# Kernel optimization log

Measured on AMD Instinct MI355X. Metric: run time of the kernel, lower is better.

The kernel has to match this reference:

```python
import jax, jax.numpy as jnp
import numpy as np


def dense_image_warp(img, flow):
    """Faithful port of tfa.image.dense_image_warp(img, flow):
    output[b,i,j] = bilinear_sample(img[b], (i - flow[b,i,j,0], j - flow[b,i,j,1]))
    with floors clamped to [0, size-2] and alphas clipped to [0,1] (TFA semantics).
    """
    B, H, W, C = img.shape
    gy = jnp.arange(H, dtype=flow.dtype)[None, :, None]   # [1,H,1]
    gx = jnp.arange(W, dtype=flow.dtype)[None, None, :]   # [1,1,W]
    # query = grid - flow
    qy = gy - flow[..., 0]                                 # [B,H,W]
    qx = gx - flow[..., 1]
    fy = jnp.clip(jnp.floor(qy), 0.0, H - 2)
    fx = jnp.clip(jnp.floor(qx), 0.0, W - 2)
    ay = jnp.clip(qy - fy, 0.0, 1.0)[..., None]            # [B,H,W,1]
    ax = jnp.clip(qx - fx, 0.0, 1.0)[..., None]
    fy_i = fy.astype(jnp.int32)
    fx_i = fx.astype(jnp.int32)

    flat = img.reshape(B, H * W, C)

    def gather(yy, xx):  # yy,xx: [B,H,W] int32
        idx = (yy * W + xx).reshape(B, H * W, 1)
        return jnp.take_along_axis(flat, idx, axis=1).reshape(B, H, W, C)

    tl = gather(fy_i,     fx_i)
    tr = gather(fy_i,     fx_i + 1)
    bl = gather(fy_i + 1, fx_i)
    br = gather(fy_i + 1, fx_i + 1)

    top = tl + (tr - tl) * ax
    bot = bl + (br - bl) * ax
    return top + (bot - top) * ay


def setup_inputs() -> dict:
    key = jax.random.key(0)
    k1, k2 = jax.random.split(key)
    img = jax.random.normal(k1, (16, 256, 512, 32), dtype=jnp.float32)
    flow = jax.random.normal(k2, (16, 256, 512, 2), dtype=jnp.float32)
    return {"img": img, "flow": flow}


def reference(img, flow):
    # InvWarpFlow.call: dense_image_warp(img, -flow)
    return dense_image_warp(img, -flow)
```

## Files before the change

kernel.cpp:

```cpp
#include <hip/hip_runtime.h>


__global__ __launch_bounds__(256) void InvWarpFlow_kernel(
    const float* __restrict__ img,
    const float* __restrict__ flow,
    float* __restrict__ out)
{
    constexpr int H = 256, W = 512, C = 32;
    int t   = blockIdx.x * blockDim.x + threadIdx.x;
    int cg  = t & 7;
    int pix = t >> 3;
    int x   = pix & (W - 1);
    int yb  = pix >> 9;
    int y   = yb & (H - 1);
    int b   = yb >> 8;

    const float2 f = *reinterpret_cast<const float2*>(flow + (size_t)pix * 2);
    float qy = (float)y + f.x;
    float qx = (float)x + f.y;

    float fy = fminf(fmaxf(floorf(qy), 0.0f), (float)(H - 2));
    float fx = fminf(fmaxf(floorf(qx), 0.0f), (float)(W - 2));
    float ay = fminf(fmaxf(qy - fy, 0.0f), 1.0f);
    float ax = fminf(fmaxf(qx - fx, 0.0f), 1.0f);
    int iy = (int)fy;
    int ix = (int)fx;

    const float* base = img + ((((size_t)b * H + iy) * W + ix) * C) + cg * 4;
    float4 tl = *reinterpret_cast<const float4*>(base);
    float4 tr = *reinterpret_cast<const float4*>(base + C);
    float4 bl = *reinterpret_cast<const float4*>(base + (size_t)W * C);
    float4 br = *reinterpret_cast<const float4*>(base + (size_t)W * C + C);

    float4 o;
    {
        float top, bot;
        top = tl.x + (tr.x - tl.x) * ax;
        bot = bl.x + (br.x - bl.x) * ax;
        o.x = top + (bot - top) * ay;
        top = tl.y + (tr.y - tl.y) * ax;
        bot = bl.y + (br.y - bl.y) * ax;
        o.y = top + (bot - top) * ay;
        top = tl.z + (tr.z - tl.z) * ax;
        bot = bl.z + (br.z - bl.z) * ax;
        o.z = top + (bot - top) * ay;
        top = tl.w + (tr.w - tl.w) * ax;
        bot = bl.w + (br.w - bl.w) * ax;
        o.w = top + (bot - top) * ay;
    }

    *reinterpret_cast<float4*>(out + (size_t)pix * C + cg * 4) = o;
}

extern "C" void kernel_launch(void* const* d_in, const int* in_sizes, int n_in,
                              void* d_out, int out_size, void* d_ws, size_t ws_size,
                              hipStream_t stream) {
    const float* img  = (const float*)d_in[0];
    const float* flow = (const float*)d_in[1];
    float* out = (float*)d_out;

    constexpr int B = 16, H = 256, W = 512;
    int total_threads = B * H * W * 8;
    int block = 256;
    int grid  = total_threads / block;
    InvWarpFlow_kernel<<<grid, block, 0, stream>>>(img, flow, out);
}
```

Measured before the change: 114.6 us.

## Tile pixels into 8x8 blocks with XCD-aware block remapping and nontemporal stores

```diff
diff --git a/kernel.cpp b/kernel.cpp
--- a/kernel.cpp
+++ b/kernel.cpp
@@ -1,19 +1,37 @@
 #include <hip/hip_runtime.h>
 
 
-__global__ __launch_bounds__(256) void InvWarpFlow_kernel(
+typedef float floatx4 __attribute__((ext_vector_type(4)));
+
+__global__ __launch_bounds__(512) void InvWarpFlow_kernel(
     const float* __restrict__ img,
     const float* __restrict__ flow,
     float* __restrict__ out)
 {
     constexpr int H = 256, W = 512, C = 32;
-    int t   = blockIdx.x * blockDim.x + threadIdx.x;
-    int cg  = t & 7;
-    int pix = t >> 3;
-    int x   = pix & (W - 1);
-    int yb  = pix >> 9;
-    int y   = yb & (H - 1);
-    int b   = yb >> 8;
+    constexpr int TW = 8, TH = 8;
+    constexpr int TILES_Y = H / TH;
+    constexpr int TILES_X = W / TW;
+    constexpr int NBLK = 16 * TILES_X * TILES_Y;
+    constexpr int PER_XCD = NBLK / 8;
+
+    int bid = blockIdx.x;
+    int logical = (bid & 7) * PER_XCD + (bid >> 3);
+
+    int ty   = logical & (TILES_Y - 1);
+    int rest = logical >> 5;
+    int tx   = rest & (TILES_X - 1);
+    int b    = rest >> 6;
+
+    int t  = threadIdx.x;
+    int cg = t & 7;
+    int p  = t >> 3;
+    int lx = p & 7;
+    int ly = p >> 3;
+
+    int x = tx * TW + lx;
+    int y = ty * TH + ly;
+    int pix = ((b << 8) + y) * W + x;
 
     const float2 f = *reinterpret_cast<const float2*>(flow + (size_t)pix * 2);
     float qy = (float)y + f.x;
@@ -27,29 +45,16 @@
     int ix = (int)fx;
 
     const float* base = img + ((((size_t)b * H + iy) * W + ix) * C) + cg * 4;
-    float4 tl = *reinterpret_cast<const float4*>(base);
-    float4 tr = *reinterpret_cast<const float4*>(base + C);
-    float4 bl = *reinterpret_cast<const float4*>(base + (size_t)W * C);
-    float4 br = *reinterpret_cast<const float4*>(base + (size_t)W * C + C);
+    floatx4 tl = *reinterpret_cast<const floatx4*>(base);
+    floatx4 tr = *reinterpret_cast<const floatx4*>(base + C);
+    floatx4 bl = *reinterpret_cast<const floatx4*>(base + (size_t)W * C);
+    floatx4 br = *reinterpret_cast<const floatx4*>(base + (size_t)W * C + C);
 
-    float4 o;
-    {
-        float top, bot;
-        top = tl.x + (tr.x - tl.x) * ax;
-        bot = bl.x + (br.x - bl.x) * ax;
-        o.x = top + (bot - top) * ay;
-        top = tl.y + (tr.y - tl.y) * ax;
-        bot = bl.y + (br.y - bl.y) * ax;
-        o.y = top + (bot - top) * ay;
-        top = tl.z + (tr.z - tl.z) * ax;
-        bot = bl.z + (br.z - bl.z) * ax;
-        o.z = top + (bot - top) * ay;
-        top = tl.w + (tr.w - tl.w) * ax;
-        bot = bl.w + (br.w - bl.w) * ax;
-        o.w = top + (bot - top) * ay;
-    }
+    floatx4 top = tl + (tr - tl) * ax;
+    floatx4 bot = bl + (br - bl) * ax;
+    floatx4 o   = top + (bot - top) * ay;
 
-    *reinterpret_cast<float4*>(out + (size_t)pix * C + cg * 4) = o;
+    __builtin_nontemporal_store(o, reinterpret_cast<floatx4*>(out + (size_t)pix * C + cg * 4));
 }
 
 extern "C" void kernel_launch(void* const* d_in, const int* in_sizes, int n_in,
@@ -59,9 +64,6 @@
     const float* flow = (const float*)d_in[1];
     float* out = (float*)d_out;
 
-    constexpr int B = 16, H = 256, W = 512;
-    int total_threads = B * H * W * 8;
-    int block = 256;
-    int grid  = total_threads / block;
-    InvWarpFlow_kernel<<<grid, block, 0, stream>>>(img, flow, out);
+    constexpr int NBLK = 32768;
+    InvWarpFlow_kernel<<<NBLK, 512, 0, stream>>>(img, flow, out);
 }
```

Result: slower. 117.3 us (+2.3%).
